# Kernel optimization log

Hardware: AMD Instinct MI355X
Metric: run time of the kernel (lower is better)

The kernel has to match this reference:

```python
import jax, jax.numpy as jnp
import numpy as np

B, N, T, D, H = 4, 8, 512, 256, 8
DK = D // H


def _dwconv(x, w, b=None):
    # x: (BN, D, T) depthwise conv, kernel 3, padding 'same', groups=D
    y = jax.lax.conv_general_dilated(
        x, w, window_strides=(1,), padding='SAME',
        feature_group_count=x.shape[1],
        dimension_numbers=('NCH', 'OIH', 'NCH'))
    if b is not None:
        y = y + b[None, :, None]
    return y


def setup_inputs() -> dict:
    key = jax.random.key(0)
    ks = jax.random.split(key, 16)
    s = 1.0 / np.sqrt(D)
    s3 = 1.0 / np.sqrt(3 * D)
    inp = {
        'query': jax.random.normal(ks[0], (B, N, T, D), jnp.float32),
        'key': jax.random.normal(ks[1], (B, N, T, D), jnp.float32),
        'value': jax.random.normal(ks[2], (B, N, T, D), jnp.float32),
        'key_padding_mask': jax.random.randint(ks[3], (B, N, T), 0, 2, jnp.int32),
        # depthwise conv params
        'w_pos': jax.random.uniform(ks[4], (D, 1, 3), jnp.float32, -0.577, 0.577),
        'b_pos': jax.random.uniform(ks[5], (D,), jnp.float32, -0.577, 0.577),
        # physics-initialized differential operators (still learnable floats)
        'w_vel': jnp.tile(jnp.array([-1.0, 0.0, 1.0], jnp.float32)[None, None, :], (D, 1, 1)),
        'w_acc': jnp.tile(jnp.array([1.0, -2.0, 1.0], jnp.float32)[None, None, :], (D, 1, 1)),
        # fusion / projection linears (stored as (in, out))
        'Wq': jax.random.uniform(ks[6], (3 * D, D), jnp.float32, -s3, s3),
        'bq': jax.random.uniform(ks[7], (D,), jnp.float32, -s3, s3),
        'Wk': jax.random.uniform(ks[8], (3 * D, D), jnp.float32, -s3, s3),
        'bk': jax.random.uniform(ks[9], (D,), jnp.float32, -s3, s3),
        'Wv': jax.random.uniform(ks[10], (D, D), jnp.float32, -s, s),
        'bv': jax.random.uniform(ks[11], (D,), jnp.float32, -s, s),
        'Wo': jax.random.uniform(ks[12], (D, D), jnp.float32, -s, s),
        'bo': jax.random.uniform(ks[13], (D,), jnp.float32, -s, s),
    }
    return inp


def reference(query, key, value, key_padding_mask,
              w_pos, b_pos, w_vel, w_acc,
              Wq, bq, Wk, bk, Wv, bv, Wo, bo):
    b, n, t, d = query.shape
    scale = jnp.float32(1.0 / np.sqrt(DK))

    def kin_feats(x):
        xin = x.reshape(b * n, t, d).transpose(0, 2, 1)  # (BN, D, T)
        p = _dwconv(xin, w_pos, b_pos)
        v = _dwconv(xin, w_vel)
        a = _dwconv(xin, w_acc)
        return jnp.concatenate([p, v, a], axis=1).transpose(0, 2, 1)  # (BN, T, 3D)

    qc = kin_feats(query)
    kc = kin_feats(key)

    Q = (qc @ Wq + bq).reshape(b, n, t, H, DK).transpose(0, 1, 3, 2, 4)  # (B,N,H,Tq,dk)
    K = (kc @ Wk + bk).reshape(b, n, t, H, DK).transpose(0, 1, 3, 2, 4)
    V = (value @ Wv + bv).reshape(b, n, t, H, DK).transpose(0, 1, 3, 2, 4)

    scores = jnp.einsum('bnhqd,bnhkd->bnhqk', Q, K) * scale
    mask = key_padding_mask.astype(bool)[:, :, None, None, :]  # (B,N,1,1,Tk)
    scores = jnp.where(mask, jnp.float32(-1e9), scores)
    attn = jax.nn.softmax(scores, axis=-1)  # dropout is identity in eval

    ctx = jnp.einsum('bnhqk,bnhkd->bnhqd', attn, V)
    ctx = ctx.transpose(0, 1, 3, 2, 4).reshape(b, n, t, d)
    return ctx @ Wo + bo
```

## Files before the change

### kernel.cpp

```cpp
#include <hip/hip_runtime.h>
#include <math.h>


typedef __attribute__((ext_vector_type(8))) short bf16x8;
typedef __attribute__((ext_vector_type(4))) float f32x4;
typedef __attribute__((ext_vector_type(16))) float f32x16;
typedef __attribute__((ext_vector_type(4))) int i32x4;

__device__ __forceinline__ unsigned short f2bf(float f) {
    unsigned u = __float_as_uint(f);
    return (unsigned short)((u + 0x7fff + ((u >> 16) & 1)) >> 16);
}
__device__ __forceinline__ float ex2(float x) {
    float r; asm("v_exp_f32 %0, %1" : "=v"(r) : "v"(x)); return r;
}
__device__ __forceinline__ int cvtpk(float lo, float hi) {
    int r; asm("v_cvt_pk_bf16_f32 %0, %1, %2" : "=v"(r) : "v"(lo), "v"(hi)); return r;
}
__device__ __forceinline__ void gll16(const void* gsrc, const void* ldst) {
    __builtin_amdgcn_global_load_lds(
        (const __attribute__((address_space(1))) unsigned int*)gsrc,
        (__attribute__((address_space(3))) unsigned int*)ldst, 16, 0, 0);
}

#define SCL (0.17677669529663689f * 1.4426950408889634f)

#define OFF_ZERO 0u
#define OFF_BTQ  25231360u
#define OFF_BTK  25624576u
#define OFF_BEFF 26017792u
#define OFF_WVT  26019840u
#define OFF_WOT  26150912u
#define OFF_QB   26413056u
#define OFF_KB   34801664u
#define OFF_VV   43190272u
#define OFF_CTX  51578880u

__global__ __launch_bounds__(256) void prep(
    const float* __restrict__ Wq, const float* __restrict__ Wk,
    const float* __restrict__ bq, const float* __restrict__ bk,
    const float* __restrict__ wp, const float* __restrict__ wv,
    const float* __restrict__ wa, const float* __restrict__ b_pos,
    const float* __restrict__ Wv, const float* __restrict__ Wo,
    unsigned short* __restrict__ BtQ, unsigned short* __restrict__ BtK,
    float* __restrict__ beff, unsigned short* __restrict__ WVT,
    unsigned short* __restrict__ WOT, float* __restrict__ zeropage)
{
    int bid = blockIdx.x;
    if (bid < 1536) {
        int idx = bid * 256 + threadIdx.x;
        int which = idx / 196608;
        int r = idx - which * 196608;
        int j = r >> 16;
        int rem = r & 65535;
        int n = rem >> 8;
        int d = rem & 255;
        const float* W = which ? Wk : Wq;
        float val = wp[d * 3 + j] * W[d * 256 + n]
                  + wv[d * 3 + j] * W[(256 + d) * 256 + n]
                  + wa[d * 3 + j] * W[(512 + d) * 256 + n];
        if (!which) val *= SCL;
        (which ? BtK : BtQ)[n * 768 + j * 256 + d] = f2bf(val);
    } else if (bid < 2048) {
        int idx = (bid - 1536) * 256 + threadIdx.x;
        int which = idx >> 16;
        int r = idx & 65535;
        int n = r >> 8, kk = r & 255;
        if (!which) WVT[n * 256 + kk] = f2bf(Wv[kk * 256 + n]);
        else        WOT[n * 256 + kk] = f2bf(Wo[kk * 256 + n]);
    } else if (bid < 2050) {
        int which = bid - 2048;
        int n = threadIdx.x;
        const float* W = which ? Wk : Wq;
        const float* bb = which ? bk : bq;
        float s = bb[n];
        for (int d = 0; d < 256; ++d) s = fmaf(b_pos[d], W[d * 256 + n], s);
        if (!which) s *= SCL;
        beff[which * 256 + n] = s;
    } else {
        if (threadIdx.x < 64) zeropage[threadIdx.x] = 0.f;
    }
}

template<int KTOT, bool IM2COL>
__device__ __forceinline__ void gemmf32(
    const float* __restrict__ A, const unsigned short* __restrict__ Bt,
    const float* __restrict__ bias, const float* __restrict__ zeropage,
    unsigned short* __restrict__ Out, float* Asf, unsigned short* Bs)
{
    const int tid = threadIdx.x;
    const int wid = tid >> 6, l = tid & 63;
    const int l31 = l & 31, h2 = l >> 5;
    const int wm = wid >> 1, wn = wid & 1;
    const int m0 = blockIdx.x * 128, n0 = blockIdx.y * 128;

    f32x16 acc[2][2] = {};

    for (int k0 = 0; k0 < KTOT; k0 += 64) {
        __syncthreads();
        #pragma unroll
        for (int q = 0; q < 8; ++q) {
            int cidx = q * 256 + tid;
            int row = cidx >> 4, cch = cidx & 15;
            int csrc = (cch ^ (row & 15)) * 4;
            const float* asrc;
            if constexpr (IM2COL) {
                int seq = m0 >> 9, t0 = m0 & 511;
                int st = t0 + row + (k0 >> 8) - 1;
                asrc = (st >= 0 && st < 512)
                     ? A + ((size_t)(seq * 512 + st) * 256 + (k0 & 255) + csrc)
                     : zeropage + csrc;
            } else {
                asrc = A + ((size_t)(m0 + row) * 256 + k0 + csrc);
            }
            gll16(asrc, Asf + (size_t)cidx * 4);
        }
        #pragma unroll
        for (int q = 0; q < 4; ++q) {
            int cidx = q * 256 + tid;
            int row = cidx >> 3, c = cidx & 7;
            gll16(Bt + (size_t)(n0 + row) * KTOT + k0 + ((c ^ (row & 7)) * 8),
                  Bs + cidx * 8);
        }
        __syncthreads();
        #pragma unroll
        for (int ks = 0; ks < 4; ++ks) {
            const int c = ks * 2 + h2;
            bf16x8 af[2], bfr[2];
            #pragma unroll
            for (int mt = 0; mt < 2; ++mt) {
                int r = wm * 64 + mt * 32 + l31;
                f32x4 f0 = *(const f32x4*)&Asf[r * 64 + (((2 * c) ^ (r & 15)) * 4)];
                f32x4 f1 = *(const f32x4*)&Asf[r * 64 + (((2 * c + 1) ^ (r & 15)) * 4)];
                i32x4 w = {cvtpk(f0[0], f0[1]), cvtpk(f0[2], f0[3]),
                           cvtpk(f1[0], f1[1]), cvtpk(f1[2], f1[3])};
                af[mt] = __builtin_bit_cast(bf16x8, w);
            }
            #pragma unroll
            for (int nt = 0; nt < 2; ++nt) {
                int rn = wn * 64 + nt * 32 + l31;
                bfr[nt] = *(const bf16x8*)&Bs[rn * 64 + ((c ^ (rn & 7)) * 8)];
            }
            #pragma unroll
            for (int mt = 0; mt < 2; ++mt)
                #pragma unroll
                for (int nt = 0; nt < 2; ++nt)
                    acc[mt][nt] = __builtin_amdgcn_mfma_f32_32x32x16_bf16(af[mt], bfr[nt], acc[mt][nt], 0, 0, 0);
        }
    }

    #pragma unroll
    for (int nt = 0; nt < 2; ++nt) {
        const int col = n0 + wn * 64 + nt * 32 + l31;
        const float bb = bias[col];
        #pragma unroll
        for (int mt = 0; mt < 2; ++mt) {
            #pragma unroll
            for (int r = 0; r < 16; ++r) {
                const int row = m0 + wm * 64 + mt * 32 + 4 * h2 + (r & 3) + 8 * (r >> 2);
                Out[(size_t)row * 256 + col] = f2bf(acc[mt][nt][r] + bb);
            }
        }
    }
}

template<int KTOT, typename OutT>
__device__ __forceinline__ void gemm97(
    const unsigned short* __restrict__ A, const unsigned short* __restrict__ Bt,
    const float* __restrict__ bias, OutT* __restrict__ Out,
    unsigned short* As, unsigned short* Bs)
{
    const int tid = threadIdx.x;
    const int wid = tid >> 6, l = tid & 63;
    const int l31 = l & 31, h2 = l >> 5;
    const int wm = wid >> 1, wn = wid & 1;
    const int m0 = blockIdx.x * 128, n0 = blockIdx.y * 128;

    f32x16 acc[2][2] = {};

    for (int k0 = 0; k0 < KTOT; k0 += 64) {
        __syncthreads();
        #pragma unroll
        for (int q = 0; q < 4; ++q) {
            int cidx = q * 256 + tid;
            int row = cidx >> 3;
            int csrc = ((cidx & 7) ^ (row & 7)) * 8;
            gll16(A + (size_t)(m0 + row) * 256 + (k0 & 255) + csrc, As + (size_t)cidx * 8);
            gll16(Bt + (size_t)(n0 + row) * KTOT + k0 + csrc, Bs + (size_t)cidx * 8);
        }
        __syncthreads();
        #pragma unroll
        for (int ks = 0; ks < 4; ++ks) {
            bf16x8 af[2], bfr[2];
            #pragma unroll
            for (int mt = 0; mt < 2; ++mt) {
                int r = wm * 64 + mt * 32 + l31;
                af[mt] = *(const bf16x8*)&As[r * 64 + (((ks * 2 + h2) ^ (r & 7)) * 8)];
            }
            #pragma unroll
            for (int nt = 0; nt < 2; ++nt) {
                int rn = wn * 64 + nt * 32 + l31;
                bfr[nt] = *(const bf16x8*)&Bs[rn * 64 + (((ks * 2 + h2) ^ (rn & 7)) * 8)];
            }
            #pragma unroll
            for (int mt = 0; mt < 2; ++mt)
                #pragma unroll
                for (int nt = 0; nt < 2; ++nt)
                    acc[mt][nt] = __builtin_amdgcn_mfma_f32_32x32x16_bf16(af[mt], bfr[nt], acc[mt][nt], 0, 0, 0);
        }
    }

    #pragma unroll
    for (int nt = 0; nt < 2; ++nt) {
        const int col = n0 + wn * 64 + nt * 32 + l31;
        const float bb = bias[col];
        #pragma unroll
        for (int mt = 0; mt < 2; ++mt) {
            #pragma unroll
            for (int r = 0; r < 16; ++r) {
                const int row = m0 + wm * 64 + mt * 32 + 4 * h2 + (r & 3) + 8 * (r >> 2);
                float v = acc[mt][nt][r] + bb;
                if constexpr (sizeof(OutT) == 2) Out[(size_t)row * 256 + col] = (OutT)f2bf(v);
                else Out[(size_t)row * 256 + col] = v;
            }
        }
    }
}

__global__ __launch_bounds__(256) void proj_fused(
    const float* __restrict__ query, const float* __restrict__ key,
    const float* __restrict__ value,
    const unsigned short* __restrict__ BTQ, const unsigned short* __restrict__ BTK,
    const unsigned short* __restrict__ WVT,
    const float* __restrict__ BEFF, const float* __restrict__ bv,
    const float* __restrict__ zeropage,
    unsigned short* __restrict__ QB, unsigned short* __restrict__ KB,
    unsigned short* __restrict__ VV)
{
    __shared__ alignas(16) float Asf[8192];
    __shared__ alignas(16) unsigned short Bs[8192];
    const int z = blockIdx.z;
    if (z == 0)      gemmf32<768, true>(query, BTQ, BEFF, zeropage, QB, Asf, Bs);
    else if (z == 1) gemmf32<768, true>(key, BTK, BEFF + 256, zeropage, KB, Asf, Bs);
    else             gemmf32<256, false>(value, WVT, bv, zeropage, VV, Asf, Bs);
}

__global__ __launch_bounds__(256) void outproj(
    const unsigned short* __restrict__ CTX, const unsigned short* __restrict__ WOT,
    const float* __restrict__ bo, float* __restrict__ Out)
{
    __shared__ alignas(16) unsigned short As[8192];
    __shared__ alignas(16) unsigned short Bs[8192];
    gemm97<256, float>(CTX, WOT, bo, Out, As, Bs);
}

__global__ __launch_bounds__(512) void attn_mfma(const unsigned short* __restrict__ Qb,
                                                 const unsigned short* __restrict__ Kb,
                                                 const unsigned short* __restrict__ Vv,
                                                 const int* __restrict__ mask,
                                                 unsigned short* __restrict__ ctx) {
    __shared__ alignas(16) unsigned short Ks[2][128 * 32];
    __shared__ alignas(16) unsigned short VsT[2][32 * 136];
    __shared__ float Mb[2][128];

    const int bnh = blockIdx.x;
    const int bn = bnh >> 3, h = bnh & 7;
    const int tid = threadIdx.x, wid = tid >> 6, l = tid & 63;
    const int g = l >> 4, r15 = l & 15;
    const unsigned short* Qg = Qb + (size_t)bn * 512 * 256 + h * 32;
    const unsigned short* Kg = Kb + (size_t)bn * 512 * 256 + h * 32;
    const unsigned short* Vg = Vv + (size_t)bn * 512 * 256 + h * 32;
    const int* mp = mask + bn * 512;
    const int srow = tid >> 2;
    const int vkey = tid & 127, vd0 = (tid >> 7) * 8;

    auto stageK = [&](int k0, int b) {
        int csrc = (((tid & 3) ^ (srow & 3))) * 8;
        gll16(Kg + ((size_t)(k0 + srow)) * 256 + csrc, &Ks[b][wid * 512]);
    };

    bf16x8 bq[4];
    #pragma unroll
    for (int qt = 0; qt < 4; ++qt)
        bq[qt] = *(const bf16x8*)(const void*)(Qg + ((size_t)(qt * 128 + wid * 16 + r15)) * 256 + g * 8);

    stageK(0, 0);
    {
        i32x4 vr = *(const i32x4*)(const void*)(Vg + (size_t)vkey * 256 + vd0);
        #pragma unroll
        for (int i = 0; i < 4; ++i) {
            unsigned u = (unsigned)vr[i];
            VsT[0][(vd0 + 2 * i) * 136 + vkey] = (unsigned short)(u & 0xffff);
            VsT[0][(vd0 + 2 * i + 1) * 136 + vkey] = (unsigned short)(u >> 16);
        }
        if (tid < 128) Mb[0][tid] = (mp[tid] != 0) ? -1e9f : 0.f;
    }
    __syncthreads();

    float mrun[4], lrun[4];
    f32x4 accO[4][2] = {};
    #pragma unroll
    for (int qt = 0; qt < 4; ++qt) { mrun[qt] = -1e30f; lrun[qt] = 0.f; }

    for (int kt = 0; kt < 4; ++kt) {
        const int cur = kt & 1, nxt = cur ^ 1;
        const int k0n = kt * 128 + 128;

        i32x4 vr;
        int mraw = 0;
        if (kt < 3) {
            stageK(k0n, nxt);
            vr = *(const i32x4*)(const void*)(Vg + ((size_t)(k0n + vkey)) * 256 + vd0);
            if (tid < 128) mraw = mp[k0n + tid];
        }

        bf16x8 av[2][4];
        #pragma unroll
        for (int mt = 0; mt < 2; ++mt)
            #pragma unroll
            for (int s = 0; s < 4; ++s)
                av[mt][s] = *(const bf16x8*)&VsT[cur][(mt * 16 + r15) * 136 + 32 * s + 8 * g];

        #pragma unroll
        for (int qt = 0; qt < 4; ++qt) {
            float p[8][4];
            float rmax = -3e38f;
            __builtin_amdgcn_s_setprio(1);
            #pragma unroll
            for (int t2 = 0; t2 < 8; ++t2) {
                const int base = 32 * (t2 >> 1) + 4 * (t2 & 1);
                const int arow = base + 8 * (r15 >> 2) + (r15 & 3);
                bf16x8 ak = *(const bf16x8*)&Ks[cur][arow * 32 + ((g ^ (arow & 3)) * 8)];
                f32x4 cin = *(const f32x4*)&Mb[cur][base + 8 * g];
                f32x4 st = __builtin_amdgcn_mfma_f32_16x16x32_bf16(ak, bq[qt], cin, 0, 0, 0);
                #pragma unroll
                for (int r = 0; r < 4; ++r) p[t2][r] = st[r];
                rmax = fmaxf(rmax, fmaxf(fmaxf(st[0], st[1]), fmaxf(st[2], st[3])));
            }
            __builtin_amdgcn_s_setprio(0);
            rmax = fmaxf(rmax, __shfl_xor(rmax, 16, 64));
            rmax = fmaxf(rmax, __shfl_xor(rmax, 32, 64));

            if (__ballot(rmax > mrun[qt])) {
                float mnew = fmaxf(mrun[qt], rmax);
                float fs = ex2(mrun[qt] - mnew);
                lrun[qt] *= fs;
                accO[qt][0] *= fs;
                accO[qt][1] *= fs;
                mrun[qt] = mnew;
            }
            float psum = 0.f;
            #pragma unroll
            for (int t2 = 0; t2 < 8; ++t2)
                #pragma unroll
                for (int r = 0; r < 4; ++r) {
                    float e = ex2(p[t2][r] - mrun[qt]);
                    p[t2][r] = e;
                    psum += e;
                }
            psum += __shfl_xor(psum, 16, 64);
            psum += __shfl_xor(psum, 32, 64);
            lrun[qt] += psum;

            bf16x8 pb[4];
            #pragma unroll
            for (int s = 0; s < 4; ++s) {
                i32x4 bi = {cvtpk(p[2 * s][0], p[2 * s][1]), cvtpk(p[2 * s][2], p[2 * s][3]),
                            cvtpk(p[2 * s + 1][0], p[2 * s + 1][1]), cvtpk(p[2 * s + 1][2], p[2 * s + 1][3])};
                pb[s] = __builtin_bit_cast(bf16x8, bi);
            }

            __builtin_amdgcn_s_setprio(1);
            #pragma unroll
            for (int mt = 0; mt < 2; ++mt)
                #pragma unroll
                for (int s = 0; s < 4; ++s)
                    accO[qt][mt] = __builtin_amdgcn_mfma_f32_16x16x32_bf16(av[mt][s], pb[s], accO[qt][mt], 0, 0, 0);
            __builtin_amdgcn_s_setprio(0);
        }

        if (kt < 3) {
            #pragma unroll
            for (int i = 0; i < 4; ++i) {
                unsigned u = (unsigned)vr[i];
                VsT[nxt][(vd0 + 2 * i) * 136 + vkey] = (unsigned short)(u & 0xffff);
                VsT[nxt][(vd0 + 2 * i + 1) * 136 + vkey] = (unsigned short)(u >> 16);
            }
            if (tid < 128) Mb[nxt][tid] = (mraw != 0) ? -1e9f : 0.f;
        }
        __syncthreads();
    }

    #pragma unroll
    for (int qt = 0; qt < 4; ++qt) {
        const float inv = 1.f / lrun[qt];
        const size_t orow = (size_t)bn * 512 + qt * 128 + wid * 16 + r15;
        #pragma unroll
        for (int mt = 0; mt < 2; ++mt) {
            ushort4 o;
            o.x = f2bf(accO[qt][mt][0] * inv);
            o.y = f2bf(accO[qt][mt][1] * inv);
            o.z = f2bf(accO[qt][mt][2] * inv);
            o.w = f2bf(accO[qt][mt][3] * inv);
            *(ushort4*)&ctx[orow * 256 + h * 32 + mt * 16 + 4 * g] = o;
        }
    }
}

extern "C" void kernel_launch(void* const* d_in, const int* in_sizes, int n_in,
                              void* d_out, int out_size, void* d_ws, size_t ws_size,
                              hipStream_t stream) {
    const float* query = (const float*)d_in[0];
    const float* key   = (const float*)d_in[1];
    const float* value = (const float*)d_in[2];
    const int*   kpm   = (const int*)d_in[3];
    const float* w_pos = (const float*)d_in[4];
    const float* b_pos = (const float*)d_in[5];
    const float* w_vel = (const float*)d_in[6];
    const float* w_acc = (const float*)d_in[7];
    const float* Wq    = (const float*)d_in[8];
    const float* bq    = (const float*)d_in[9];
    const float* Wk    = (const float*)d_in[10];
    const float* bk    = (const float*)d_in[11];
    const float* Wv    = (const float*)d_in[12];
    const float* bv    = (const float*)d_in[13];
    const float* Wo    = (const float*)d_in[14];
    const float* bo    = (const float*)d_in[15];

    unsigned char* w = (unsigned char*)d_ws;
    float*          ZP  = (float*)(w + OFF_ZERO);
    unsigned short* BTQ = (unsigned short*)(w + OFF_BTQ);
    unsigned short* BTK = (unsigned short*)(w + OFF_BTK);
    float*          BEFF= (float*)(w + OFF_BEFF);
    unsigned short* WVT = (unsigned short*)(w + OFF_WVT);
    unsigned short* WOT = (unsigned short*)(w + OFF_WOT);
    unsigned short* QB  = (unsigned short*)(w + OFF_QB);
    unsigned short* KB  = (unsigned short*)(w + OFF_KB);
    unsigned short* VV  = (unsigned short*)(w + OFF_VV);
    unsigned short* CTX = (unsigned short*)(w + OFF_CTX);

    prep<<<2051, 256, 0, stream>>>(Wq, Wk, bq, bk, w_pos, w_vel, w_acc, b_pos,
                                   Wv, Wo, BTQ, BTK, BEFF, WVT, WOT, ZP);

    proj_fused<<<dim3(128, 2, 3), 256, 0, stream>>>(query, key, value, BTQ, BTK, WVT,
                                                    BEFF, bv, ZP, QB, KB, VV);

    attn_mfma<<<256, 512, 0, stream>>>(QB, KB, VV, kpm, CTX);

    outproj<<<dim3(128, 2), 256, 0, stream>>>(CTX, WOT, bo, (float*)d_out);
}
```

Baseline: 80.54 us.

## Reuse halo-extended A tile across conv taps and double-buffer B tiles

The implicit-im2col projection GEMM now loads one 130-row fp32 A tile per 64-channel block and reuses it for all three temporal taps by shifting the row index, instead of reloading a shifted A tile for every tap. B tiles for the next tap are prefetched into a second LDS buffer while the current tap computes, which removes one barrier pair per tap. This cuts A global traffic and barriers for Q/K projections. In exchange LDS use rises (extra halo rows and a second B buffer), which may reduce occupancy, and the shifted row reads may change LDS bank-conflict behaviour.

After: 79.17 us (median of 2 runs). About the same (-1.7%).

```diff
diff --git a/kernel.cpp b/kernel.cpp
--- a/kernel.cpp
+++ b/kernel.cpp
@@ -82,54 +82,64 @@
     }
 }
 
-template<int KTOT, bool IM2COL>
+template<int TAPS>
 __device__ __forceinline__ void gemmf32(
     const float* __restrict__ A, const unsigned short* __restrict__ Bt,
     const float* __restrict__ bias, const float* __restrict__ zeropage,
     unsigned short* __restrict__ Out, float* Asf, unsigned short* Bs)
 {
+    constexpr int KTOT = TAPS * 256;
+    constexpr int ROWS_A = (TAPS > 1) ? 130 : 128;
+    constexpr int NCHUNK_A = ROWS_A * 16;
     const int tid = threadIdx.x;
     const int wid = tid >> 6, l = tid & 63;
     const int l31 = l & 31, h2 = l >> 5;
     const int wm = wid >> 1, wn = wid & 1;
     const int m0 = blockIdx.x * 128, n0 = blockIdx.y * 128;
+    const int seq = m0 >> 9, t0 = m0 & 511;
 
     f32x16 acc[2][2] = {};
 
-    for (int k0 = 0; k0 < KTOT; k0 += 64) {
-        __syncthreads();
-        #pragma unroll
-        for (int q = 0; q < 8; ++q) {
+    auto stageA = [&](int cb) {
+        const int c0 = cb * 64;
+        #pragma unroll
+        for (int q = 0; q < (NCHUNK_A + 255) / 256; ++q) {
             int cidx = q * 256 + tid;
-            int row = cidx >> 4, cch = cidx & 15;
-            int csrc = (cch ^ (row & 15)) * 4;
-            const float* asrc;
-            if constexpr (IM2COL) {
-                int seq = m0 >> 9, t0 = m0 & 511;
-                int st = t0 + row + (k0 >> 8) - 1;
-                asrc = (st >= 0 && st < 512)
-                     ? A + ((size_t)(seq * 512 + st) * 256 + (k0 & 255) + csrc)
-                     : zeropage + csrc;
-            } else {
-                asrc = A + ((size_t)(m0 + row) * 256 + k0 + csrc);
-            }
-            gll16(asrc, Asf + (size_t)cidx * 4);
-        }
+            if (cidx < NCHUNK_A) {
+                int row = cidx >> 4, cch = cidx & 15;
+                int csrc = (cch ^ (row & 15)) * 4;
+                const float* asrc;
+                if constexpr (TAPS > 1) {
+                    int st = t0 + row - 1;
+                    asrc = (st >= 0 && st < 512)
+                         ? A + ((size_t)(seq * 512 + st) * 256 + c0 + csrc)
+                         : zeropage + csrc;
+                } else {
+                    asrc = A + ((size_t)(m0 + row) * 256 + c0 + csrc);
+                }
+                gll16(asrc, Asf + (size_t)cidx * 4);
+            }
+        }
+    };
+    auto stageB = [&](int cb, int tap, int b) {
+        const int kbase = tap * 256 + cb * 64;
         #pragma unroll
         for (int q = 0; q < 4; ++q) {
             int cidx = q * 256 + tid;
             int row = cidx >> 3, c = cidx & 7;
-            gll16(Bt + (size_t)(n0 + row) * KTOT + k0 + ((c ^ (row & 7)) * 8),
-                  Bs + cidx * 8);
-        }
-        __syncthreads();
+            gll16(Bt + (size_t)(n0 + row) * KTOT + kbase + ((c ^ (row & 7)) * 8),
+                  Bs + b * 8192 + cidx * 8);
+        }
+    };
+    auto compute = [&](int tap, int b) {
+        const unsigned short* bs = Bs + b * 8192;
         #pragma unroll
         for (int ks = 0; ks < 4; ++ks) {
             const int c = ks * 2 + h2;
             bf16x8 af[2], bfr[2];
             #pragma unroll
             for (int mt = 0; mt < 2; ++mt) {
-                int r = wm * 64 + mt * 32 + l31;
+                int r = wm * 64 + mt * 32 + l31 + tap;
                 f32x4 f0 = *(const f32x4*)&Asf[r * 64 + (((2 * c) ^ (r & 15)) * 4)];
                 f32x4 f1 = *(const f32x4*)&Asf[r * 64 + (((2 * c + 1) ^ (r & 15)) * 4)];
                 i32x4 w = {cvtpk(f0[0], f0[1]), cvtpk(f0[2], f0[3]),
@@ -139,13 +149,28 @@
             #pragma unroll
             for (int nt = 0; nt < 2; ++nt) {
                 int rn = wn * 64 + nt * 32 + l31;
-                bfr[nt] = *(const bf16x8*)&Bs[rn * 64 + ((c ^ (rn & 7)) * 8)];
+                bfr[nt] = *(const bf16x8*)&bs[rn * 64 + ((c ^ (rn & 7)) * 8)];
             }
             #pragma unroll
             for (int mt = 0; mt < 2; ++mt)
                 #pragma unroll
                 for (int nt = 0; nt < 2; ++nt)
                     acc[mt][nt] = __builtin_amdgcn_mfma_f32_32x32x16_bf16(af[mt], bfr[nt], acc[mt][nt], 0, 0, 0);
+        }
+    };
+
+    int buf = 0;
+    #pragma unroll
+    for (int cb = 0; cb < 4; ++cb) {
+        if (cb) __syncthreads();
+        stageA(cb);
+        stageB(cb, 0, buf);
+        __syncthreads();
+        #pragma unroll
+        for (int tap = 0; tap < TAPS; ++tap) {
+            if (tap + 1 < TAPS) stageB(cb, tap + 1, buf ^ 1);
+            compute(tap, buf);
+            if (tap + 1 < TAPS) { __syncthreads(); buf ^= 1; }
         }
     }
 
@@ -237,12 +262,12 @@
     unsigned short* __restrict__ QB, unsigned short* __restrict__ KB,
     unsigned short* __restrict__ VV)
 {
-    __shared__ alignas(16) float Asf[8192];
-    __shared__ alignas(16) unsigned short Bs[8192];
+    __shared__ alignas(16) float Asf[130 * 64];
+    __shared__ alignas(16) unsigned short Bs[2 * 8192];
     const int z = blockIdx.z;
-    if (z == 0)      gemmf32<768, true>(query, BTQ, BEFF, zeropage, QB, Asf, Bs);
-    else if (z == 1) gemmf32<768, true>(key, BTK, BEFF + 256, zeropage, KB, Asf, Bs);
-    else             gemmf32<256, false>(value, WVT, bv, zeropage, VV, Asf, Bs);
+    if (z == 0)      gemmf32<3>(query, BTQ, BEFF, zeropage, QB, Asf, Bs);
+    else if (z == 1) gemmf32<3>(key, BTK, BEFF + 256, zeropage, KB, Asf, Bs);
+    else             gemmf32<1>(value, WVT, bv, zeropage, VV, Asf, Bs);
 }
 
 __global__ __launch_bounds__(256) void outproj(
```
